# Optimization experiments

Hardware: AMD Instinct MI355X
Metric: run time of the kernel (lower is better)

The kernel has to match this reference:

```python
import jax, jax.numpy as jnp
import numpy as np

EPS = 1e-12   # F.normalize default eps
TH = 0.5      # forward-arg default threshold
CLAMP_LO, CLAMP_HI = 0.01, 0.999


def setup_inputs() -> dict:
    key = jax.random.key(0)
    k1, k2 = jax.random.split(key)
    # x4: ResNet layer3 features after ala1 scaling + upfeat, stride-16 of a 1024px image
    x4 = jax.random.normal(k1, (8, 1024, 64, 64), dtype=jnp.float32)
    # logits: classifier output after upfeat, same spatial grid, 21 classes
    logits = jax.random.normal(k2, (8, 21, 64, 64), dtype=jnp.float32)
    return {"x4": x4, "logits": logits, "pcm": 2}


def reference(x4, logits, pcm):
    b, c, h, w = x4.shape
    hw = h * w
    xf = x4.reshape(b, c, hw)                      # [b, c, hw]
    # F.normalize(dim=1): x / max(||x||_2, eps)
    norm = jnp.sqrt(jnp.sum(xf * xf, axis=1, keepdims=True))
    xn = xf / jnp.maximum(norm, EPS)
    # pixel affinity: [b, hw, hw]
    aff = jnp.einsum('bci,bcj->bij', xn, xn)
    aff = jnp.clip(aff, CLAMP_LO, CLAMP_HI)
    aff = jnp.where(aff < TH, jnp.zeros((), aff.dtype), aff)
    # column-normalize (torch sum over dim=1)
    aff = aff / jnp.sum(aff, axis=1, keepdims=True)
    lf = logits.reshape(b, -1, hw)                 # [b, K, hw]
    for _ in range(pcm):                           # pcm is a Python int
        lf = jnp.einsum('bki,bij->bkj', lf, aff)
    return lf.reshape(b, -1, h, w)
```

## Files before the change

### kernel.cpp

```cpp
#include <hip/hip_runtime.h>
#include <hip/hip_bf16.h>

#define B_   8
#define C_   1024
#define HW_  4096
#define NK   21
#define NT   32
#define NTRI (NT * (NT + 1) / 2)

using bf16 = __hip_bfloat16;
typedef __attribute__((ext_vector_type(4))) float float4_;
typedef __attribute__((ext_vector_type(8))) int int8v;

#define WAITV0() asm volatile("s_waitcnt vmcnt(0)" ::: "memory")
#define FENCE()  asm volatile("" ::: "memory")
#define BARRIER() do { FENCE(); __builtin_amdgcn_s_barrier(); FENCE(); } while (0)

__global__ __launch_bounds__(256) void ktrans(const float* __restrict__ x4, float* __restrict__ sumsq,
                                              unsigned char* __restrict__ Xq) {
    int jt = blockIdx.x, b = blockIdx.y;
    int j0 = jt * 64;
    int t = threadIdx.x;
    __shared__ float tin[128][33];
    __shared__ unsigned int outw[32][260];
    __shared__ float ssq[32];

    int jl = t & 31, cl = t >> 5;
    int qq = t >> 5, jq = t & 31;

    for (int jg = 0; jg < 2; ++jg) {
        int jbase = j0 + jg * 32;
        if (t < 32) ssq[t] = 0.f;
        float part = 0.f;

        for (int ct = 0; ct < 8; ++ct) {
            __syncthreads();
#pragma unroll
            for (int cc = 0; cc < 16; ++cc) {
                float v = x4[((size_t)b * C_ + ct * 128 + cc * 8 + cl) * HW_ + jbase + jl];
                tin[cc * 8 + cl][jl] = v;
                part = fmaf(v, v, part);
            }
            __syncthreads();
            unsigned int wv[4];
#pragma unroll
            for (int g = 0; g < 4; ++g) {
                float f0 = tin[qq * 16 + g * 4 + 0][jq];
                float f1 = tin[qq * 16 + g * 4 + 1][jq];
                float f2 = tin[qq * 16 + g * 4 + 2][jq];
                float f3 = tin[qq * 16 + g * 4 + 3][jq];
                unsigned int r = 0;
                r = __builtin_amdgcn_cvt_pk_fp8_f32(f0, f1, r, false);
                r = __builtin_amdgcn_cvt_pk_fp8_f32(f2, f3, r, true);
                wv[g] = r;
            }
            *(uint4*)&outw[jq][ct * 32 + qq * 4] = make_uint4(wv[0], wv[1], wv[2], wv[3]);
        }
        atomicAdd(&ssq[jl], part);
        __syncthreads();

#pragma unroll
        for (int ps = 0; ps < 8; ++ps) {
            int r = ps * 4 + (t >> 6);
            int ch = t & 63;
            uint4 v = *(const uint4*)&outw[r][ch * 4];
            *(uint4*)(Xq + ((size_t)b * HW_ + jbase + r) * C_ + ch * 16) = v;
        }
        if (t < 32) sumsq[b * HW_ + jbase + t] = ssq[t];
        __syncthreads();
    }
}

__global__ __launch_bounds__(256, 2) void kgram(const unsigned char* __restrict__ Xq,
                                                const float* __restrict__ sumsq, bf16* __restrict__ aff,
                                                float* __restrict__ colsum, int* __restrict__ flags) {
    int lin = blockIdx.x;
    int b = lin & 7;
    int p = lin >> 3;
    int it = (int)((2.0f * NT + 1.0f - sqrtf((2.0f * NT + 1.0f) * (2.0f * NT + 1.0f) - 8.0f * (float)p)) * 0.5f);
    while (it > 0 && p < it * NT - it * (it - 1) / 2) --it;
    while (p >= (it + 1) * NT - (it + 1) * it / 2) ++it;
    int jt = it + p - (it * NT - it * (it - 1) / 2);

    int i0 = it * 128, j0 = jt * 128;
    int tid = threadIdx.x, w = tid >> 6, l = tid & 63;
    int wr = w >> 1, wc = w & 1;
    int lrow = l & 15, lk = l >> 4;

    __shared__ __align__(16) unsigned char smem[2][32768];
    __shared__ int fl;

    const unsigned char* XA = Xq + ((size_t)b * HW_ + i0) * C_;
    const unsigned char* XB = Xq + ((size_t)b * HW_ + j0) * C_;

    int rhi = tid >> 3, sl = tid & 7;

    auto stg = [&](unsigned char* buf, int k0) {
#pragma unroll
        for (int q = 0; q < 4; ++q) {
            int R = q * 32 + rhi;
            int gp = sl ^ (R & 7);
            __builtin_amdgcn_global_load_lds(
                (const __attribute__((address_space(1))) void*)(XA + (size_t)R * C_ + k0 + (gp << 4)),
                (__attribute__((address_space(3))) void*)(buf + R * 128 + (sl << 4)), 16, 0, 0);
            __builtin_amdgcn_global_load_lds(
                (const __attribute__((address_space(1))) void*)(XB + (size_t)R * C_ + k0 + (gp << 4)),
                (__attribute__((address_space(3))) void*)(buf + 16384 + R * 128 + (sl << 4)), 16, 0, 0);
        }
    };

    auto ldfrag = [&](const unsigned char* base, int r) {
        int sw = r & 7;
        uint4 lo = *(const uint4*)(base + r * 128 + (((lk * 2) ^ sw) << 4));
        uint4 hi = *(const uint4*)(base + r * 128 + (((lk * 2 + 1) ^ sw) << 4));
        int8v v; v[0] = lo.x; v[1] = lo.y; v[2] = lo.z; v[3] = lo.w;
        v[4] = hi.x; v[5] = hi.y; v[6] = hi.z; v[7] = hi.w;
        return v;
    };

    float4_ acc[4][4];
#pragma unroll
    for (int m = 0; m < 4; ++m)
#pragma unroll
        for (int n = 0; n < 4; ++n) acc[m][n] = {0.f, 0.f, 0.f, 0.f};

    stg(smem[0], 0);
    WAITV0();
    BARRIER();

    for (int kt = 0; kt < 8; ++kt) {
        unsigned char* cur = smem[kt & 1];
        if (kt < 7) stg(smem[(kt + 1) & 1], (kt + 1) * 128);

        int8v bv[4];
#pragma unroll
        for (int n = 0; n < 4; ++n) bv[n] = ldfrag(cur + 16384, wc * 64 + n * 16 + lrow);
        __builtin_amdgcn_s_setprio(1);
#pragma unroll
        for (int m = 0; m < 4; ++m) {
            int8v av = ldfrag(cur, wr * 64 + m * 16 + lrow);
#pragma unroll
            for (int n = 0; n < 4; ++n)
                acc[m][n] = __builtin_amdgcn_mfma_scale_f32_16x16x128_f8f6f4(
                    av, bv[n], acc[m][n], 0, 0, 0, 0x7f7f7f7f, 0, 0x7f7f7f7f);
        }
        __builtin_amdgcn_s_setprio(0);

        if (kt < 7) WAITV0();
        BARRIER();
    }

    float rnj[4];
#pragma unroll
    for (int n = 0; n < 4; ++n) {
        int j = j0 + wc * 64 + n * 16 + lrow;
        rnj[n] = 1.0f / fmaxf(sqrtf(sumsq[b * HW_ + j]), 1e-12f);
    }
    float rni[4][4];
#pragma unroll
    for (int m = 0; m < 4; ++m)
#pragma unroll
        for (int r = 0; r < 4; ++r) {
            int i = i0 + wr * 64 + m * 16 + lk * 4 + r;
            rni[m][r] = 1.0f / fmaxf(sqrtf(sumsq[b * HW_ + i]), 1e-12f);
        }
    bool any = false;
#pragma unroll
    for (int m = 0; m < 4; ++m)
#pragma unroll
        for (int n = 0; n < 4; ++n)
#pragma unroll
            for (int r = 0; r < 4; ++r) {
                acc[m][n][r] *= rni[m][r] * rnj[n];
                any |= (acc[m][n][r] >= 0.5f);
            }

    if (tid == 0) fl = 0;
    __syncthreads();
    unsigned long long bal = __ballot(any);
    if (l == 0 && bal != 0ull) atomicOr(&fl, 1);
    __syncthreads();
    bool mirror = (it != jt);
    if (tid == 0) {
        flags[(b * NT + it) * NT + jt] = fl;
        if (mirror) flags[(b * NT + jt) * NT + it] = fl;
    }

    if (fl) {
        size_t affb = (size_t)b * HW_ * HW_;
        float rsum[4][4];
#pragma unroll
        for (int m = 0; m < 4; ++m)
#pragma unroll
            for (int r = 0; r < 4; ++r) rsum[m][r] = 0.f;

#pragma unroll
        for (int n = 0; n < 4; ++n) {
            int j = j0 + wc * 64 + n * 16 + lrow;
            float cs = 0.f;
#pragma unroll
            for (int m = 0; m < 4; ++m) {
#pragma unroll
                for (int r = 0; r < 4; ++r) {
                    float v = acc[m][n][r];
                    v = fminf(fmaxf(v, 0.01f), 0.999f);
                    v = (v < 0.5f) ? 0.0f : v;
                    bf16 bb = __float2bfloat16(v);
                    int i = i0 + wr * 64 + m * 16 + lk * 4 + r;
                    aff[affb + (size_t)i * HW_ + j] = bb;
                    float bf = __bfloat162float(bb);
                    cs += bf;
                    rsum[m][r] += bf;
                    if (mirror) aff[affb + (size_t)j * HW_ + i] = bb;
                }
            }
            cs += __shfl_xor(cs, 16);
            cs += __shfl_xor(cs, 32);
            if (lk == 0) atomicAdd(&colsum[b * HW_ + j], cs);
        }
        if (mirror) {
#pragma unroll
            for (int m = 0; m < 4; ++m) {
#pragma unroll
                for (int r = 0; r < 4; ++r) {
                    float s = rsum[m][r];
                    s += __shfl_xor(s, 1);
                    s += __shfl_xor(s, 2);
                    s += __shfl_xor(s, 4);
                    s += __shfl_xor(s, 8);
                    if (lrow == 0) {
                        int i = i0 + wr * 64 + m * 16 + lk * 4 + r;
                        atomicAdd(&colsum[b * HW_ + i], s);
                    }
                }
            }
        }
    }
}

__global__ __launch_bounds__(256) void kprop(const float* __restrict__ lf, const bf16* __restrict__ aff,
                                             const int* __restrict__ flags, const float* __restrict__ colsum,
                                             float* __restrict__ outp) {
    int jt = blockIdx.x, b = blockIdx.y;
    int t = threadIdx.x;
    int q = t >> 6, jl = t & 63;
    int j = jt * 64 + jl;
    __shared__ float lfs[NK * 128];
    __shared__ float ps[3][NK][64];
    float acc[NK];
#pragma unroll
    for (int k = 0; k < NK; ++k) acc[k] = 0.f;

    for (int it = 0; it < NT; ++it) {
        if (flags[(b * NT + it) * NT + (jt >> 1)] == 0) continue;
        __syncthreads();
        for (int idx = t; idx < NK * 128; idx += 256)
            lfs[idx] = lf[((size_t)b * NK + (idx >> 7)) * HW_ + it * 128 + (idx & 127)];
        __syncthreads();
        const bf16* ap = aff + ((size_t)b * HW_ + it * 128 + q * 32) * HW_ + j;
        for (int ii = 0; ii < 32; ii += 4) {
            float a0 = __bfloat162float(ap[(size_t)(ii + 0) * HW_]);
            float a1 = __bfloat162float(ap[(size_t)(ii + 1) * HW_]);
            float a2 = __bfloat162float(ap[(size_t)(ii + 2) * HW_]);
            float a3 = __bfloat162float(ap[(size_t)(ii + 3) * HW_]);
            int base = (q * 32 + ii);
#pragma unroll
            for (int k = 0; k < NK; ++k)
                acc[k] = fmaf(lfs[(k << 7) + base + 0], a0,
                          fmaf(lfs[(k << 7) + base + 1], a1,
                          fmaf(lfs[(k << 7) + base + 2], a2,
                          fmaf(lfs[(k << 7) + base + 3], a3, acc[k]))));
        }
    }

    if (q) {
#pragma unroll
        for (int k = 0; k < NK; ++k) ps[q - 1][k][jl] = acc[k];
    }
    __syncthreads();
    if (q == 0) {
        float inv = 1.0f / colsum[b * HW_ + j];
#pragma unroll
        for (int k = 0; k < NK; ++k) {
            float s = acc[k] + ps[0][k][jl] + ps[1][k][jl] + ps[2][k][jl];
            outp[((size_t)b * NK + k) * HW_ + j] = s * inv;
        }
    }
}

extern "C" void kernel_launch(void* const* d_in, const int* in_sizes, int n_in,
                              void* d_out, int out_size, void* d_ws, size_t ws_size,
                              hipStream_t stream) {
    const float* x4 = (const float*)d_in[0];
    const float* logits = (const float*)d_in[1];
    float* out = (float*)d_out;

    char* w = (char*)d_ws;
    size_t off = 0;
    auto take = [&](size_t bytes) {
        char* p = w + off;
        off += (bytes + 255) & ~(size_t)255;
        return p;
    };
    unsigned char* Xq = (unsigned char*)take((size_t)B_ * HW_ * C_);
    bf16* aff     = (bf16*)take((size_t)B_ * HW_ * HW_ * 2);
    float* colsum = (float*)take((size_t)B_ * HW_ * 4);
    int*   flags  = (int*)take((size_t)B_ * NT * NT * 4);
    float* sumsq  = (float*)take((size_t)B_ * HW_ * 4);
    float* lf1    = (float*)take((size_t)B_ * NK * HW_ * 4);

    hipMemsetAsync(colsum, 0,
                   (size_t)B_ * HW_ * 4 + (size_t)B_ * NT * NT * 4, stream);

    ktrans<<<dim3(64, B_), dim3(256), 0, stream>>>(x4, sumsq, Xq);
    kgram <<<dim3(NTRI * B_), dim3(256), 0, stream>>>(Xq, sumsq, aff, colsum, flags);

    kprop<<<dim3(64, B_), dim3(256), 0, stream>>>(logits, aff, flags, colsum, lf1);
    kprop<<<dim3(64, B_), dim3(256), 0, stream>>>(lf1, aff, flags, colsum, out);
}
```

Before: 338.1 us.

## Fuse both propagation steps into one kernel and drop the workspace memset

Replaces the two kprop launches with one kprop2 kernel over 128-column tiles. For each nonzero row tile it recomputes the matching intermediate lf1 tile, using the tile-sparsity flags, and applies it at once. This removes the intermediate lf1 buffer, one launch, and the global round trip. The hipMemsetAsync is dropped and colsum is now zeroed inside ktrans. The cost is redundant recomputation of lf1 tiles across column blocks, which is cheap only when the affinity is very sparse. Flags are no longer explicitly cleared, which may be unsafe if kgram does not write every entry.

```diff
diff --git a/kernel.cpp b/kernel.cpp
--- a/kernel.cpp
+++ b/kernel.cpp
@@ -17,13 +17,15 @@
 #define BARRIER() do { FENCE(); __builtin_amdgcn_s_barrier(); FENCE(); } while (0)
 
 __global__ __launch_bounds__(256) void ktrans(const float* __restrict__ x4, float* __restrict__ sumsq,
-                                              unsigned char* __restrict__ Xq) {
+                                              unsigned char* __restrict__ Xq, float* __restrict__ colsum) {
     int jt = blockIdx.x, b = blockIdx.y;
     int j0 = jt * 64;
     int t = threadIdx.x;
     __shared__ float tin[128][33];
     __shared__ unsigned int outw[32][260];
     __shared__ float ssq[32];
+
+    if (t < 64) colsum[b * HW_ + j0 + t] = 0.f;
 
     int jl = t & 31, cl = t >> 5;
     int qq = t >> 5, jq = t & 31;
@@ -238,53 +240,89 @@
     }
 }
 
-__global__ __launch_bounds__(256) void kprop(const float* __restrict__ lf, const bf16* __restrict__ aff,
-                                             const int* __restrict__ flags, const float* __restrict__ colsum,
-                                             float* __restrict__ outp) {
+__global__ __launch_bounds__(256) void kprop2(const float* __restrict__ lf, const bf16* __restrict__ aff,
+                                              const int* __restrict__ flags, const float* __restrict__ colsum,
+                                              float* __restrict__ outp) {
     int jt = blockIdx.x, b = blockIdx.y;
     int t = threadIdx.x;
-    int q = t >> 6, jl = t & 63;
-    int j = jt * 64 + jl;
+    int q = t >> 7, jl = t & 127;
+    int j = jt * 128 + jl;
     __shared__ float lfs[NK * 128];
-    __shared__ float ps[3][NK][64];
-    float acc[NK];
-#pragma unroll
-    for (int k = 0; k < NK; ++k) acc[k] = 0.f;
+    __shared__ float lf1t[NK * 128];
+
+    float oacc[NK];
+#pragma unroll
+    for (int k = 0; k < NK; ++k) oacc[k] = 0.f;
 
     for (int it = 0; it < NT; ++it) {
-        if (flags[(b * NT + it) * NT + (jt >> 1)] == 0) continue;
-        __syncthreads();
-        for (int idx = t; idx < NK * 128; idx += 256)
-            lfs[idx] = lf[((size_t)b * NK + (idx >> 7)) * HW_ + it * 128 + (idx & 127)];
-        __syncthreads();
-        const bf16* ap = aff + ((size_t)b * HW_ + it * 128 + q * 32) * HW_ + j;
-        for (int ii = 0; ii < 32; ii += 4) {
-            float a0 = __bfloat162float(ap[(size_t)(ii + 0) * HW_]);
-            float a1 = __bfloat162float(ap[(size_t)(ii + 1) * HW_]);
-            float a2 = __bfloat162float(ap[(size_t)(ii + 2) * HW_]);
-            float a3 = __bfloat162float(ap[(size_t)(ii + 3) * HW_]);
-            int base = (q * 32 + ii);
+        if (flags[(b * NT + it) * NT + jt] == 0) continue;
+
+        float racc[NK];
+#pragma unroll
+        for (int k = 0; k < NK; ++k) racc[k] = 0.f;
+
+        for (int ht = 0; ht < NT; ++ht) {
+            if (flags[(b * NT + ht) * NT + it] == 0) continue;
+            __syncthreads();
+            for (int idx = t; idx < NK * 128; idx += 256)
+                lfs[idx] = lf[((size_t)b * NK + (idx >> 7)) * HW_ + ht * 128 + (idx & 127)];
+            __syncthreads();
+            const bf16* ap = aff + ((size_t)b * HW_ + ht * 128 + q * 64) * HW_ + it * 128 + jl;
+            for (int ii = 0; ii < 64; ii += 4) {
+                float a0 = __bfloat162float(ap[(size_t)(ii + 0) * HW_]);
+                float a1 = __bfloat162float(ap[(size_t)(ii + 1) * HW_]);
+                float a2 = __bfloat162float(ap[(size_t)(ii + 2) * HW_]);
+                float a3 = __bfloat162float(ap[(size_t)(ii + 3) * HW_]);
+                int base = q * 64 + ii;
+#pragma unroll
+                for (int k = 0; k < NK; ++k)
+                    racc[k] = fmaf(lfs[(k << 7) + base + 0], a0,
+                               fmaf(lfs[(k << 7) + base + 1], a1,
+                               fmaf(lfs[(k << 7) + base + 2], a2,
+                               fmaf(lfs[(k << 7) + base + 3], a3, racc[k]))));
+            }
+        }
+        __syncthreads();
+        if (q == 1) {
+#pragma unroll
+            for (int k = 0; k < NK; ++k) lfs[(k << 7) + jl] = racc[k];
+        }
+        __syncthreads();
+        if (q == 0) {
+            float invi = 1.0f / colsum[b * HW_ + it * 128 + jl];
 #pragma unroll
             for (int k = 0; k < NK; ++k)
-                acc[k] = fmaf(lfs[(k << 7) + base + 0], a0,
-                          fmaf(lfs[(k << 7) + base + 1], a1,
-                          fmaf(lfs[(k << 7) + base + 2], a2,
-                          fmaf(lfs[(k << 7) + base + 3], a3, acc[k]))));
-        }
-    }
-
-    if (q) {
-#pragma unroll
-        for (int k = 0; k < NK; ++k) ps[q - 1][k][jl] = acc[k];
+                lf1t[(k << 7) + jl] = (racc[k] + lfs[(k << 7) + jl]) * invi;
+        }
+        __syncthreads();
+
+        const bf16* ap2 = aff + ((size_t)b * HW_ + it * 128 + q * 64) * HW_ + j;
+        for (int ii = 0; ii < 64; ii += 4) {
+            float a0 = __bfloat162float(ap2[(size_t)(ii + 0) * HW_]);
+            float a1 = __bfloat162float(ap2[(size_t)(ii + 1) * HW_]);
+            float a2 = __bfloat162float(ap2[(size_t)(ii + 2) * HW_]);
+            float a3 = __bfloat162float(ap2[(size_t)(ii + 3) * HW_]);
+            int base = q * 64 + ii;
+#pragma unroll
+            for (int k = 0; k < NK; ++k)
+                oacc[k] = fmaf(lf1t[(k << 7) + base + 0], a0,
+                           fmaf(lf1t[(k << 7) + base + 1], a1,
+                           fmaf(lf1t[(k << 7) + base + 2], a2,
+                           fmaf(lf1t[(k << 7) + base + 3], a3, oacc[k]))));
+        }
+    }
+
+    __syncthreads();
+    if (q == 1) {
+#pragma unroll
+        for (int k = 0; k < NK; ++k) lfs[(k << 7) + jl] = oacc[k];
     }
     __syncthreads();
     if (q == 0) {
         float inv = 1.0f / colsum[b * HW_ + j];
 #pragma unroll
-        for (int k = 0; k < NK; ++k) {
-            float s = acc[k] + ps[0][k][jl] + ps[1][k][jl] + ps[2][k][jl];
-            outp[((size_t)b * NK + k) * HW_ + j] = s * inv;
-        }
+        for (int k = 0; k < NK; ++k)
+            outp[((size_t)b * NK + k) * HW_ + j] = (oacc[k] + lfs[(k << 7) + jl]) * inv;
     }
 }
 
@@ -307,14 +345,8 @@
     float* colsum = (float*)take((size_t)B_ * HW_ * 4);
     int*   flags  = (int*)take((size_t)B_ * NT * NT * 4);
     float* sumsq  = (float*)take((size_t)B_ * HW_ * 4);
-    float* lf1    = (float*)take((size_t)B_ * NK * HW_ * 4);
-
-    hipMemsetAsync(colsum, 0,
-                   (size_t)B_ * HW_ * 4 + (size_t)B_ * NT * NT * 4, stream);
-
-    ktrans<<<dim3(64, B_), dim3(256), 0, stream>>>(x4, sumsq, Xq);
+
+    ktrans<<<dim3(64, B_), dim3(256), 0, stream>>>(x4, sumsq, Xq, colsum);
     kgram <<<dim3(NTRI * B_), dim3(256), 0, stream>>>(Xq, sumsq, aff, colsum, flags);
-
-    kprop<<<dim3(64, B_), dim3(256), 0, stream>>>(logits, aff, flags, colsum, lf1);
-    kprop<<<dim3(64, B_), dim3(256), 0, stream>>>(lf1, aff, flags, colsum, out);
+    kprop2<<<dim3(NT, B_), dim3(256), 0, stream>>>(logits, aff, flags, colsum, out);
 }
```

Measured after the change: 336.5 us. No clear change (-0.5%).
